# Kernel optimization log

Hardware: AMD Instinct MI355X
Metric: run time of the kernel (lower is better)

## Reference

```python
import jax, jax.numpy as jnp
import numpy as np

N_NODES = 50000
N_EDGES = 800000


def setup_inputs() -> dict:
    key = jax.random.key(0)
    ks = jax.random.split(key, 6)
    x = jax.random.normal(ks[0], (N_NODES, 22), dtype=jnp.float32)
    # small weight scale to keep tanh in its linear-ish regime
    W0 = jax.random.normal(ks[1], (22, 220), dtype=jnp.float32) * 0.1
    W1 = jax.random.normal(ks[2], (220, 220), dtype=jnp.float32) * 0.05
    W2 = jax.random.normal(ks[3], (220, 220), dtype=jnp.float32) * 0.05
    W3 = jax.random.normal(ks[4], (220, 10), dtype=jnp.float32) * 0.05
    b0 = jnp.zeros((220,), jnp.float32)
    b1 = jnp.zeros((220,), jnp.float32)
    b2 = jnp.zeros((220,), jnp.float32)
    b3 = jnp.zeros((10,), jnp.float32)
    edge_index = jax.random.randint(ks[5], (2, N_EDGES), 0, N_NODES, dtype=jnp.int64)
    return {"x": x, "W0": W0, "b0": b0, "W1": W1, "b1": b1,
            "W2": W2, "b2": b2, "W3": W3, "b3": b3, "edge_index": edge_index}


def _graph_conv(h, W, b, src, dst, inv_sqrt_out, inv_sqrt_in, activation):
    # DGL GraphConv, norm='both':
    #   h' = D_in^{-1/2} * A^T * (D_out^{-1/2} * h) @ W + b
    h = h * inv_sqrt_out[:, None]          # [N, F_in]
    m = h[src]                             # gather: [E, F_in]
    agg = jax.ops.segment_sum(m, dst, num_segments=N_NODES)  # scatter-add: [N, F_in]
    agg = agg * inv_sqrt_in[:, None]
    out = agg @ W + b
    if activation is not None:
        out = activation(out)
    return out


def reference(x, W0, b0, W1, b1, W2, b2, W3, b3, edge_index):
    src, dst = edge_index[0], edge_index[1]
    ones = jnp.ones((edge_index.shape[1],), jnp.float32)
    deg_out = jax.ops.segment_sum(ones, src, num_segments=N_NODES)
    deg_in = jax.ops.segment_sum(ones, dst, num_segments=N_NODES)
    inv_sqrt_out = jax.lax.rsqrt(jnp.maximum(deg_out, 1.0))
    inv_sqrt_in = jax.lax.rsqrt(jnp.maximum(deg_in, 1.0))

    h = _graph_conv(x, W0, b0, src, dst, inv_sqrt_out, inv_sqrt_in, jnp.tanh)
    h = _graph_conv(h, W1, b1, src, dst, inv_sqrt_out, inv_sqrt_in, jnp.tanh)
    h = _graph_conv(h, W2, b2, src, dst, inv_sqrt_out, inv_sqrt_in, jnp.tanh)
    h = _graph_conv(h, W3, b3, src, dst, inv_sqrt_out, inv_sqrt_in, None)
    return h
```

## Files before the change

kernel.cpp:

```cpp
#include <hip/hip_runtime.h>
#include <math.h>

#define N_NODES 50000
#define N_EDGES 800000
#define NPAD 50176
#define HSTR 224

typedef __attribute__((ext_vector_type(8))) short short8;
typedef __attribute__((ext_vector_type(4))) float f32x4;
typedef __attribute__((ext_vector_type(4))) _Float16 half4;


__device__ __forceinline__ float fast_tanh(float x) {
    float e = __expf(2.0f * x);
    float r = __builtin_amdgcn_rcpf(e + 1.0f);
    return 1.0f - 2.0f * r;
}

__device__ __forceinline__ unsigned short rne_bf16(float x) {
    unsigned u = __builtin_bit_cast(unsigned, x);
    return (unsigned short)((u + 0x7FFFu + ((u >> 16) & 1u)) >> 16);
}

__device__ __forceinline__ void split_bf16(float x, unsigned short& hi, unsigned short& lo) {
    hi = rne_bf16(x);
    float hf = __builtin_bit_cast(float, (unsigned)hi << 16);
    lo = rne_bf16(x - hf);
}

__device__ __forceinline__ f32x4 mfma16(short8 a, short8 b, f32x4 c) {
    return __builtin_amdgcn_mfma_f32_16x16x32_bf16(a, b, c, 0, 0, 0);
}

__device__ __forceinline__ void wsplit_one(const float* __restrict__ W, int KIN, int LDA,
                                           unsigned short* __restrict__ WT_hi,
                                           unsigned short* __restrict__ WT_lo, int idx) {
    int n = idx / LDA;
    int k = idx - n * LDA;
    float v = (n < 220 && k < KIN) ? W[k * 220 + n] : 0.f;
    unsigned short hi, lo;
    split_bf16(v, hi, lo);
    WT_hi[idx] = hi;
    WT_lo[idx] = lo;
}


__global__ void k_hist_wsplit(const int* __restrict__ ei, int* __restrict__ deg_out,
                              int* __restrict__ ecsbuf, int* __restrict__ rank,
                              const float* __restrict__ W0, const float* __restrict__ W1,
                              const float* __restrict__ W2,
                              unsigned short* __restrict__ wt0h, unsigned short* __restrict__ wt0l,
                              unsigned short* __restrict__ wt1h, unsigned short* __restrict__ wt1l,
                              unsigned short* __restrict__ wt2h, unsigned short* __restrict__ wt2l) {
    int bx = blockIdx.x;
    if (bx < 3125) {
        int e = bx * 256 + threadIdx.x;
        if (e < N_EDGES) {
            atomicAdd(&deg_out[ei[e]], 1);
            rank[e] = atomicAdd(&ecsbuf[1 + ei[N_EDGES + e]], 1);
        }
    } else if (bx < 3153) {
        int idx = (bx - 3125) * 256 + threadIdx.x;
        if (idx < 224 * 32) wsplit_one(W0, 22, 32, wt0h, wt0l, idx);
    } else if (bx < 3349) {
        int idx = (bx - 3153) * 256 + threadIdx.x;
        wsplit_one(W1, 220, 224, wt1h, wt1l, idx);
    } else {
        int idx = (bx - 3349) * 256 + threadIdx.x;
        wsplit_one(W2, 220, 224, wt2h, wt2l, idx);
    }
}

__global__ void k_scan1(const int* __restrict__ in, int* __restrict__ out,
                        int* __restrict__ bsum, int n) {
    __shared__ int s[256];
    int i = blockIdx.x * 256 + threadIdx.x;
    int v = (i < n) ? in[i] : 0;
    s[threadIdx.x] = v;
    __syncthreads();
    for (int off = 1; off < 256; off <<= 1) {
        int t = (threadIdx.x >= off) ? s[threadIdx.x - off] : 0;
        __syncthreads();
        s[threadIdx.x] += t;
        __syncthreads();
    }
    if (i < n) out[i] = s[threadIdx.x] - v;
    if (threadIdx.x == 255 && bsum) bsum[blockIdx.x] = s[255];
}

__global__ void k_scan_mid(int* __restrict__ a, int n) {
    __shared__ int s[256];
    __shared__ int carry;
    if (threadIdx.x == 0) carry = 0;
    for (int base = 0; base < n; base += 256) {
        int i = base + threadIdx.x;
        int v = (i < n) ? a[i] : 0;
        s[threadIdx.x] = v;
        __syncthreads();
        for (int off = 1; off < 256; off <<= 1) {
            int t = (threadIdx.x >= off) ? s[threadIdx.x - off] : 0;
            __syncthreads();
            s[threadIdx.x] += t;
            __syncthreads();
        }
        int c = carry;
        if (i < n) a[i] = s[threadIdx.x] - v + c;
        __syncthreads();
        if (threadIdx.x == 0) carry = c + s[255];
        __syncthreads();
    }
}

__global__ void k_scan3(int* __restrict__ out, const int* __restrict__ bscan, int n) {
    int i = blockIdx.x * 256 + threadIdx.x;
    if (i < n) out[i] += bscan[blockIdx.x];
}

__global__ void k_post_scan(const int* __restrict__ ei, const int* __restrict__ ecsbuf,
                            const int* __restrict__ rank, const int* __restrict__ deg_out,
                            const float* __restrict__ x,
                            float* __restrict__ inv_out, float* __restrict__ inv_in,
                            int* __restrict__ src_sorted, float* __restrict__ xs) {
    int bx = blockIdx.x;
    if (bx < 196) {
        int n = bx * 256 + threadIdx.x;
        if (n >= N_NODES) return;
        int di = ecsbuf[n + 2] - ecsbuf[n + 1];
        int a = deg_out[n]; if (a < 1) a = 1;
        if (di < 1) di = 1;
        inv_out[n] = 1.0f / sqrtf((float)a);
        inv_in[n]  = 1.0f / sqrtf((float)di);
    } else if (bx < 3321) {
        int e = (bx - 196) * 256 + threadIdx.x;
        if (e < N_EDGES) {
            int d = ei[N_EDGES + e];
            src_sorted[ecsbuf[1 + d] + rank[e]] = ei[e];
        }
    } else {
        int idx = (bx - 3321) * 256 + threadIdx.x;
        if (idx >= N_NODES * 11) return;
        int n = idx / 11;
        int f2 = idx - n * 11;
        int a = deg_out[n]; if (a < 1) a = 1;
        float sc = 1.0f / sqrtf((float)a);
        float2 v = *(const float2*)&x[n * 22 + f2 * 2];
        v.x *= sc; v.y *= sc;
        *(float2*)&xs[n * 22 + f2 * 2] = v;
    }
}


__global__ void k_agg22_split(const float* __restrict__ xs,
                              const int* __restrict__ ecsbuf, const int* __restrict__ srcs,
                              const float* __restrict__ inv_in,
                              unsigned short* __restrict__ A_hi, unsigned short* __restrict__ A_lo) {
    int idx = blockIdx.x * 256 + threadIdx.x;
    int n = idx >> 4, f2 = idx & 15;
    if (n >= N_NODES) return;
    float ax = 0.f, ay = 0.f;
    if (f2 <= 10) {
        const float2* xb = (const float2*)(xs) + f2;
        int e = ecsbuf[n + 1], end = ecsbuf[n + 2];
        for (; e + 3 < end; e += 4) {
            int s0 = srcs[e], s1 = srcs[e + 1], s2 = srcs[e + 2], s3 = srcs[e + 3];
            float2 v0 = xb[s0 * 11], v1 = xb[s1 * 11];
            float2 v2 = xb[s2 * 11], v3 = xb[s3 * 11];
            ax += (v0.x + v1.x) + (v2.x + v3.x);
            ay += (v0.y + v1.y) + (v2.y + v3.y);
        }
        for (; e < end; ++e) {
            float2 v0 = xb[srcs[e] * 11];
            ax += v0.x;
            ay += v0.y;
        }
        float si = inv_in[n];
        ax *= si; ay *= si;
    }
    ushort2 h2, l2;
    split_bf16(ax, h2.x, l2.x);
    split_bf16(ay, h2.y, l2.y);
    *(ushort2*)&A_hi[n * 32 + f2 * 2] = h2;
    *(ushort2*)&A_lo[n * 32 + f2 * 2] = l2;
}

__global__ __launch_bounds__(256) void k_agg220_split(const _Float16* __restrict__ h,
                                                      const int* __restrict__ ecsbuf,
                                                      const int* __restrict__ srcs,
                                                      const float* __restrict__ inv_in,
                                                      unsigned short* __restrict__ A_hi,
                                                      unsigned short* __restrict__ A_lo) {
    int lane = threadIdx.x & 63;
    int n = blockIdx.x * 4 + (threadIdx.x >> 6);
    if (n >= N_NODES || lane >= 56) return;
    size_t ob = (size_t)n * 224 + lane * 4;
    if (lane == 55) {
        ushort4 z = {0, 0, 0, 0};
        *(ushort4*)&A_hi[ob] = z;
        *(ushort4*)&A_lo[ob] = z;
        return;
    }
    int f4 = lane * 4;
    const _Float16* hb = h + f4;
    int e = ecsbuf[n + 1], end = ecsbuf[n + 2];
    float4 a0 = {0,0,0,0}, a1 = {0,0,0,0}, a2 = {0,0,0,0}, a3 = {0,0,0,0};
    for (; e + 7 < end; e += 8) {
        int s0 = srcs[e],     s1 = srcs[e + 1], s2 = srcs[e + 2], s3 = srcs[e + 3];
        int s4 = srcs[e + 4], s5 = srcs[e + 5], s6 = srcs[e + 6], s7 = srcs[e + 7];
        half4 v0 = *(const half4*)(hb + (size_t)s0 * HSTR);
        half4 v1 = *(const half4*)(hb + (size_t)s1 * HSTR);
        half4 v2 = *(const half4*)(hb + (size_t)s2 * HSTR);
        half4 v3 = *(const half4*)(hb + (size_t)s3 * HSTR);
        half4 v4 = *(const half4*)(hb + (size_t)s4 * HSTR);
        half4 v5 = *(const half4*)(hb + (size_t)s5 * HSTR);
        half4 v6 = *(const half4*)(hb + (size_t)s6 * HSTR);
        half4 v7 = *(const half4*)(hb + (size_t)s7 * HSTR);
        a0.x += (float)v0.x; a0.y += (float)v0.y; a0.z += (float)v0.z; a0.w += (float)v0.w;
        a1.x += (float)v1.x; a1.y += (float)v1.y; a1.z += (float)v1.z; a1.w += (float)v1.w;
        a2.x += (float)v2.x; a2.y += (float)v2.y; a2.z += (float)v2.z; a2.w += (float)v2.w;
        a3.x += (float)v3.x; a3.y += (float)v3.y; a3.z += (float)v3.z; a3.w += (float)v3.w;
        a0.x += (float)v4.x; a0.y += (float)v4.y; a0.z += (float)v4.z; a0.w += (float)v4.w;
        a1.x += (float)v5.x; a1.y += (float)v5.y; a1.z += (float)v5.z; a1.w += (float)v5.w;
        a2.x += (float)v6.x; a2.y += (float)v6.y; a2.z += (float)v6.z; a2.w += (float)v6.w;
        a3.x += (float)v7.x; a3.y += (float)v7.y; a3.z += (float)v7.z; a3.w += (float)v7.w;
    }
    for (; e + 3 < end; e += 4) {
        int s0 = srcs[e], s1 = srcs[e + 1], s2 = srcs[e + 2], s3 = srcs[e + 3];
        half4 v0 = *(const half4*)(hb + (size_t)s0 * HSTR);
        half4 v1 = *(const half4*)(hb + (size_t)s1 * HSTR);
        half4 v2 = *(const half4*)(hb + (size_t)s2 * HSTR);
        half4 v3 = *(const half4*)(hb + (size_t)s3 * HSTR);
        a0.x += (float)v0.x; a0.y += (float)v0.y; a0.z += (float)v0.z; a0.w += (float)v0.w;
        a1.x += (float)v1.x; a1.y += (float)v1.y; a1.z += (float)v1.z; a1.w += (float)v1.w;
        a2.x += (float)v2.x; a2.y += (float)v2.y; a2.z += (float)v2.z; a2.w += (float)v2.w;
        a3.x += (float)v3.x; a3.y += (float)v3.y; a3.z += (float)v3.z; a3.w += (float)v3.w;
    }
    for (; e < end; ++e) {
        half4 v = *(const half4*)(hb + (size_t)srcs[e] * HSTR);
        a0.x += (float)v.x; a0.y += (float)v.y; a0.z += (float)v.z; a0.w += (float)v.w;
    }
    float sc = inv_in[n];
    float4 t;
    t.x = ((a0.x + a1.x) + (a2.x + a3.x)) * sc;
    t.y = ((a0.y + a1.y) + (a2.y + a3.y)) * sc;
    t.z = ((a0.z + a1.z) + (a2.z + a3.z)) * sc;
    t.w = ((a0.w + a1.w) + (a2.w + a3.w)) * sc;
    ushort4 h4, l4;
    split_bf16(t.x, h4.x, l4.x);
    split_bf16(t.y, h4.y, l4.y);
    split_bf16(t.z, h4.z, l4.z);
    split_bf16(t.w, h4.w, l4.w);
    *(ushort4*)&A_hi[ob] = h4;
    *(ushort4*)&A_lo[ob] = l4;
}

__global__ void k_agg10_epi(const float* __restrict__ tmp, const int* __restrict__ ecsbuf,
                            const int* __restrict__ srcs, const float* __restrict__ inv_in,
                            const float* __restrict__ bias, float* __restrict__ out) {
    int idx = blockIdx.x * 256 + threadIdx.x;
    if (idx >= N_NODES * 5) return;
    int n = idx / 5;
    int f2 = idx - n * 5;
    const float2* tb = (const float2*)(tmp) + f2;
    float ax = 0.f, ay = 0.f;
    int e = ecsbuf[n + 1], end = ecsbuf[n + 2];
    for (; e + 1 < end; e += 2) {
        float2 v0 = tb[srcs[e] * 5];
        float2 v1 = tb[srcs[e + 1] * 5];
        ax += v0.x + v1.x;
        ay += v0.y + v1.y;
    }
    if (e < end) {
        float2 v0 = tb[srcs[e] * 5];
        ax += v0.x;
        ay += v0.y;
    }
    float si = inv_in[n];
    float2 o;
    o.x = ax * si + bias[f2 * 2];
    o.y = ay * si + bias[f2 * 2 + 1];
    *(float2*)&out[n * 10 + f2 * 2] = o;
}

template <int KSTEPS, int LDA, bool FUSE_W3>
__global__ __launch_bounds__(256) void k_gemm_mfma(const unsigned short* __restrict__ A_hi,
                                                   const unsigned short* __restrict__ A_lo,
                                                   const unsigned short* __restrict__ WT_hi,
                                                   const unsigned short* __restrict__ WT_lo,
                                                   const float* __restrict__ bias,
                                                   const float* __restrict__ post,
                                                   _Float16* __restrict__ out,
                                                   const float* __restrict__ W3,
                                                   float* __restrict__ tmp) {
    int tid = threadIdx.x;
    int l = tid & 63, w = tid >> 6;
    int lrow = l & 15, q = l >> 4;
    int rt = blockIdx.x * 128 + w * 32;

    const unsigned short* pa0h = A_hi + (size_t)(rt + lrow) * LDA + q * 8;
    const unsigned short* pa0l = A_lo + (size_t)(rt + lrow) * LDA + q * 8;
    const unsigned short* pa1h = pa0h + 16 * LDA;
    const unsigned short* pa1l = pa0l + 16 * LDA;

    f32x4 acc0[14], acc1[14];
#pragma unroll
    for (int ct = 0; ct < 14; ++ct) {
        acc0[ct] = (f32x4){0.f, 0.f, 0.f, 0.f};
        acc1[ct] = (f32x4){0.f, 0.f, 0.f, 0.f};
    }

#pragma unroll
    for (int ks = 0; ks < KSTEPS; ++ks) {
        int k0 = ks * 32;
        short8 ah0 = *(const short8*)(const void*)(pa0h + k0);
        short8 al0 = *(const short8*)(const void*)(pa0l + k0);
        short8 ah1 = *(const short8*)(const void*)(pa1h + k0);
        short8 al1 = *(const short8*)(const void*)(pa1l + k0);
#pragma unroll
        for (int ct = 0; ct < 14; ++ct) {
            size_t boff = (size_t)(ct * 16 + lrow) * LDA + q * 8 + k0;
            short8 bh = *(const short8*)(const void*)(WT_hi + boff);
            short8 bl = *(const short8*)(const void*)(WT_lo + boff);
            acc0[ct] = mfma16(ah0, bh, acc0[ct]);
            acc0[ct] = mfma16(ah0, bl, acc0[ct]);
            acc0[ct] = mfma16(al0, bh, acc0[ct]);
            acc1[ct] = mfma16(ah1, bh, acc1[ct]);
            acc1[ct] = mfma16(ah1, bl, acc1[ct]);
            acc1[ct] = mfma16(al1, bh, acc1[ct]);
        }
    }

    float pv0[4], pv1[4];
#pragma unroll
    for (int r = 0; r < 4; ++r) {
        int r0 = rt + q * 4 + r;
        int r1 = r0 + 16;
        pv0[r] = (r0 < N_NODES) ? post[r0] : 0.f;
        pv1[r] = (r1 < N_NODES) ? post[r1] : 0.f;
    }

    if (!FUSE_W3) {
#pragma unroll
        for (int ct = 0; ct < 14; ++ct) {
            int col = ct * 16 + lrow;
            if (col >= 220) continue;
            float bv = bias[col];
#pragma unroll
            for (int r = 0; r < 4; ++r) {
                int r0 = rt + q * 4 + r;
                int r1 = r0 + 16;
                if (r0 < N_NODES)
                    out[(size_t)r0 * HSTR + col] = (_Float16)(pv0[r] * fast_tanh(acc0[ct][r] + bv));
                if (r1 < N_NODES)
                    out[(size_t)r1 * HSTR + col] = (_Float16)(pv1[r] * fast_tanh(acc1[ct][r] + bv));
            }
        }
    } else {
#pragma unroll
        for (int half = 0; half < 2; ++half) {
            const f32x4* acc = half ? acc1 : acc0;
            const float* pv  = half ? pv1 : pv0;
            int rbase = rt + half * 16;
            float p[4][10];
#pragma unroll
            for (int r = 0; r < 4; ++r)
#pragma unroll
                for (int j = 0; j < 10; ++j) p[r][j] = 0.f;
#pragma unroll
            for (int ct = 0; ct < 14; ++ct) {
                int col = ct * 16 + lrow;
                bool cok = col < 220;
                float bv = cok ? bias[col] : 0.f;
                float w3v[10];
                if (cok) {
                    const float2* wp = (const float2*)&W3[col * 10];
#pragma unroll
                    for (int j2 = 0; j2 < 5; ++j2) {
                        float2 t = wp[j2];
                        w3v[2 * j2] = t.x;
                        w3v[2 * j2 + 1] = t.y;
                    }
                } else {
#pragma unroll
                    for (int j = 0; j < 10; ++j) w3v[j] = 0.f;
                }
#pragma unroll
                for (int r = 0; r < 4; ++r) {
                    float h2 = pv[r] * fast_tanh(acc[ct][r] + bv);
#pragma unroll
                    for (int j = 0; j < 10; ++j) p[r][j] += h2 * w3v[j];
                }
            }
#pragma unroll
            for (int r = 0; r < 4; ++r)
#pragma unroll
                for (int j = 0; j < 10; ++j) {
                    float v = p[r][j];
                    v += __shfl_xor(v, 1, 64);
                    v += __shfl_xor(v, 2, 64);
                    v += __shfl_xor(v, 4, 64);
                    v += __shfl_xor(v, 8, 64);
                    p[r][j] = v;
                }
            if (lrow == 0) {
#pragma unroll
                for (int r = 0; r < 4; ++r) {
                    int row = rbase + q * 4 + r;
                    if (row < N_NODES) {
#pragma unroll
                        for (int j2 = 0; j2 < 5; ++j2) {
                            float2 o = {p[r][2 * j2], p[r][2 * j2 + 1]};
                            *(float2*)&tmp[(size_t)row * 10 + 2 * j2] = o;
                        }
                    }
                }
            }
        }
    }
}


extern "C" void kernel_launch(void* const* d_in, const int* in_sizes, int n_in,
                              void* d_out, int out_size, void* d_ws, size_t ws_size,
                              hipStream_t stream) {
    const float* x  = (const float*)d_in[0];
    const float* W0 = (const float*)d_in[1];
    const float* b0 = (const float*)d_in[2];
    const float* W1 = (const float*)d_in[3];
    const float* b1 = (const float*)d_in[4];
    const float* W2 = (const float*)d_in[5];
    const float* b2 = (const float*)d_in[6];
    const float* W3 = (const float*)d_in[7];
    const float* b3 = (const float*)d_in[8];
    const int*   ei = (const int*)d_in[9];
    float* out = (float*)d_out;

    int* ws = (int*)d_ws;
    int* ecsbuf     = ws + 0;
    int* deg_out    = ws + 50432;
    int* bsumA      = ws + 100608;
    float* inv_out  = (float*)(ws + 100864);
    float* inv_in   = (float*)(ws + 151040);
    int* src_sorted = ws + 201216;
    unsigned short* wt0h = (unsigned short*)(ws + 1001216);
    unsigned short* wt0l = (unsigned short*)(ws + 1004800);
    unsigned short* wt1h = (unsigned short*)(ws + 1008384);
    unsigned short* wt1l = (unsigned short*)(ws + 1033472);
    unsigned short* wt2h = (unsigned short*)(ws + 1058560);
    unsigned short* wt2l = (unsigned short*)(ws + 1083648);
    unsigned short* ahi  = (unsigned short*)(ws + 1108736);
    unsigned short* alo  = (unsigned short*)(ws + 6728448);
    _Float16* hbuf = (_Float16*)(ws + 12348160);
    float* tmp10 = (float*)(ws + 23548160);
    int* rank    = (int*)ahi;
    float* xs    = (float*)(ws + 1108736 + 3000000);

    hipMemsetAsync(ws, 0, (size_t)100608 * sizeof(int), stream);

    k_hist_wsplit<<<3545, 256, 0, stream>>>(ei, deg_out, ecsbuf, rank,
                                            W0, W1, W2, wt0h, wt0l, wt1h, wt1l, wt2h, wt2l);
    k_scan1<<<196, 256, 0, stream>>>(ecsbuf + 1, ecsbuf + 1, bsumA, NPAD);
    k_scan_mid<<<1, 256, 0, stream>>>(bsumA, 196);
    k_scan3<<<196, 256, 0, stream>>>(ecsbuf + 1, bsumA, NPAD);
    k_post_scan<<<5470, 256, 0, stream>>>(ei, ecsbuf, rank, deg_out, x,
                                          inv_out, inv_in, src_sorted, xs);

    int gemm_grid = (NPAD + 127) / 128;
    int agg_grid  = (N_NODES + 3) / 4;

    k_agg22_split<<<(N_NODES * 16 + 255) / 256, 256, 0, stream>>>(
        xs, ecsbuf, src_sorted, inv_in, ahi, alo);
    k_gemm_mfma<1, 32, false><<<gemm_grid, 256, 0, stream>>>(
        ahi, alo, wt0h, wt0l, b0, inv_out, hbuf, nullptr, nullptr);

    k_agg220_split<<<agg_grid, 256, 0, stream>>>(hbuf, ecsbuf, src_sorted, inv_in, ahi, alo);
    k_gemm_mfma<7, 224, false><<<gemm_grid, 256, 0, stream>>>(
        ahi, alo, wt1h, wt1l, b1, inv_out, hbuf, nullptr, nullptr);

    k_agg220_split<<<agg_grid, 256, 0, stream>>>(hbuf, ecsbuf, src_sorted, inv_in, ahi, alo);
    k_gemm_mfma<7, 224, true><<<gemm_grid, 256, 0, stream>>>(
        ahi, alo, wt2h, wt2l, b2, inv_out, nullptr, W3, tmp10);

    k_agg10_epi<<<(N_NODES * 5 + 255) / 256, 256, 0, stream>>>(
        tmp10, ecsbuf, src_sorted, inv_in, b3, out);
}
```

Baseline: 467.9 us.

## Stage weight tiles in double-buffered LDS for MFMA GEMM

The GEMM kernel now loads the hi/lo bf16 weight slices cooperatively into a double-buffered shared-memory tile (224 rows by 72 shorts, padded) and has each wave read B fragments from LDS. Previously every wave loaded them directly from global memory. The next k-step is prefetched into registers while the current step's MFMAs run. This is meant to cut redundant global/L2 traffic for weights across the four waves. In exchange it adds about 64KB of LDS per block, which may reduce occupancy, and a barrier per k-step.

```diff
diff --git a/kernel.cpp b/kernel.cpp
--- a/kernel.cpp
+++ b/kernel.cpp
@@ -291,6 +291,8 @@
                                                    _Float16* __restrict__ out,
                                                    const float* __restrict__ W3,
                                                    float* __restrict__ tmp) {
+    __shared__ unsigned short Bs[2][224 * 72];
+
     int tid = threadIdx.x;
     int l = tid & 63, w = tid >> 6;
     int lrow = l & 15, q = l >> 4;
@@ -301,6 +303,29 @@
     const unsigned short* pa1h = pa0h + 16 * LDA;
     const unsigned short* pa1l = pa0l + 16 * LDA;
 
+    int sr[7], sjl[7], sjo[7];
+#pragma unroll
+    for (int i = 0; i < 7; ++i) {
+        int f = tid + 256 * i;
+        sr[i] = f >> 3;
+        int j = f & 7;
+        sjl[i] = (j & 3) * 8;
+        sjo[i] = (j >> 2);
+    }
+
+    {
+        short8 sreg[7];
+#pragma unroll
+        for (int i = 0; i < 7; ++i) {
+            const unsigned short* g = (sjo[i] ? WT_lo : WT_hi) + (size_t)sr[i] * LDA + sjl[i];
+            sreg[i] = *(const short8*)(const void*)g;
+        }
+#pragma unroll
+        for (int i = 0; i < 7; ++i)
+            *(short8*)(void*)&Bs[0][sr[i] * 72 + sjo[i] * 32 + sjl[i]] = sreg[i];
+    }
+    __syncthreads();
+
     f32x4 acc0[14], acc1[14];
 #pragma unroll
     for (int ct = 0; ct < 14; ++ct) {
@@ -308,24 +333,47 @@
         acc1[ct] = (f32x4){0.f, 0.f, 0.f, 0.f};
     }
 
+    int bro = lrow * 72 + q * 8;
+
 #pragma unroll
     for (int ks = 0; ks < KSTEPS; ++ks) {
+        int cur = ks & 1;
+        bool has_next = (ks + 1 < KSTEPS);
+
+        short8 sreg[7];
+        if (has_next) {
+            int k0n = (ks + 1) * 32;
+#pragma unroll
+            for (int i = 0; i < 7; ++i) {
+                const unsigned short* g = (sjo[i] ? WT_lo : WT_hi) + (size_t)sr[i] * LDA + k0n + sjl[i];
+                sreg[i] = *(const short8*)(const void*)g;
+            }
+        }
+
         int k0 = ks * 32;
         short8 ah0 = *(const short8*)(const void*)(pa0h + k0);
         short8 al0 = *(const short8*)(const void*)(pa0l + k0);
         short8 ah1 = *(const short8*)(const void*)(pa1h + k0);
         short8 al1 = *(const short8*)(const void*)(pa1l + k0);
+
 #pragma unroll
         for (int ct = 0; ct < 14; ++ct) {
-            size_t boff = (size_t)(ct * 16 + lrow) * LDA + q * 8 + k0;
-            short8 bh = *(const short8*)(const void*)(WT_hi + boff);
-            short8 bl = *(const short8*)(const void*)(WT_lo + boff);
+            const unsigned short* bp = &Bs[cur][ct * 1152 + bro];
+            short8 bh = *(const short8*)(const void*)bp;
+            short8 bl = *(const short8*)(const void*)(bp + 32);
             acc0[ct] = mfma16(ah0, bh, acc0[ct]);
             acc0[ct] = mfma16(ah0, bl, acc0[ct]);
             acc0[ct] = mfma16(al0, bh, acc0[ct]);
             acc1[ct] = mfma16(ah1, bh, acc1[ct]);
             acc1[ct] = mfma16(ah1, bl, acc1[ct]);
             acc1[ct] = mfma16(al1, bh, acc1[ct]);
+        }
+
+        if (has_next) {
+#pragma unroll
+            for (int i = 0; i < 7; ++i)
+                *(short8*)(void*)&Bs[1 - cur][sr[i] * 72 + sjo[i] * 32 + sjl[i]] = sreg[i];
+            __syncthreads();
         }
     }
 
```

New measurement: 465.8 us. No clear change (-0.5%).

## Split GEMM tiles into column halves to cut registers and raise occupancy

Applied to the files above, without the earlier changes.

The MFMA GEMM now gives each wave one 16-row tile over half of the output columns (7 column tiles) instead of two row tiles over all 14. The grid grows fourfold and launch bounds request 4 blocks per SM. The goal is fewer accumulator registers, higher occupancy and more blocks in flight. The fused W3 epilogue now writes two partial 10-wide outputs, one per column half, into separate buffers that the final aggregation kernel sums. In exchange, each A tile is loaded twice (once per column half) and the final gather does twice as many loads.

```diff
diff --git a/kernel.cpp b/kernel.cpp
--- a/kernel.cpp
+++ b/kernel.cpp
@@ -260,19 +260,20 @@
     if (idx >= N_NODES * 5) return;
     int n = idx / 5;
     int f2 = idx - n * 5;
-    const float2* tb = (const float2*)(tmp) + f2;
+    const float2* tb0 = (const float2*)(tmp) + f2;
+    const float2* tb1 = (const float2*)(tmp + (size_t)NPAD * 10) + f2;
     float ax = 0.f, ay = 0.f;
     int e = ecsbuf[n + 1], end = ecsbuf[n + 2];
     for (; e + 1 < end; e += 2) {
-        float2 v0 = tb[srcs[e] * 5];
-        float2 v1 = tb[srcs[e + 1] * 5];
-        ax += v0.x + v1.x;
-        ay += v0.y + v1.y;
+        float2 u0 = tb0[srcs[e] * 5],     w0 = tb1[srcs[e] * 5];
+        float2 u1 = tb0[srcs[e + 1] * 5], w1 = tb1[srcs[e + 1] * 5];
+        ax += (u0.x + w0.x) + (u1.x + w1.x);
+        ay += (u0.y + w0.y) + (u1.y + w1.y);
     }
     if (e < end) {
-        float2 v0 = tb[srcs[e] * 5];
-        ax += v0.x;
-        ay += v0.y;
+        float2 u0 = tb0[srcs[e] * 5], w0 = tb1[srcs[e] * 5];
+        ax += u0.x + w0.x;
+        ay += u0.y + w0.y;
     }
     float si = inv_in[n];
     float2 o;
@@ -282,135 +283,120 @@
 }
 
 template <int KSTEPS, int LDA, bool FUSE_W3>
-__global__ __launch_bounds__(256) void k_gemm_mfma(const unsigned short* __restrict__ A_hi,
-                                                   const unsigned short* __restrict__ A_lo,
-                                                   const unsigned short* __restrict__ WT_hi,
-                                                   const unsigned short* __restrict__ WT_lo,
-                                                   const float* __restrict__ bias,
-                                                   const float* __restrict__ post,
-                                                   _Float16* __restrict__ out,
-                                                   const float* __restrict__ W3,
-                                                   float* __restrict__ tmp) {
+__global__ __launch_bounds__(256, 4) void k_gemm_mfma(const unsigned short* __restrict__ A_hi,
+                                                      const unsigned short* __restrict__ A_lo,
+                                                      const unsigned short* __restrict__ WT_hi,
+                                                      const unsigned short* __restrict__ WT_lo,
+                                                      const float* __restrict__ bias,
+                                                      const float* __restrict__ post,
+                                                      _Float16* __restrict__ out,
+                                                      const float* __restrict__ W3,
+                                                      float* __restrict__ tmp) {
     int tid = threadIdx.x;
     int l = tid & 63, w = tid >> 6;
     int lrow = l & 15, q = l >> 4;
-    int rt = blockIdx.x * 128 + w * 32;
-
-    const unsigned short* pa0h = A_hi + (size_t)(rt + lrow) * LDA + q * 8;
-    const unsigned short* pa0l = A_lo + (size_t)(rt + lrow) * LDA + q * 8;
-    const unsigned short* pa1h = pa0h + 16 * LDA;
-    const unsigned short* pa1l = pa0l + 16 * LDA;
-
-    f32x4 acc0[14], acc1[14];
-#pragma unroll
-    for (int ct = 0; ct < 14; ++ct) {
-        acc0[ct] = (f32x4){0.f, 0.f, 0.f, 0.f};
-        acc1[ct] = (f32x4){0.f, 0.f, 0.f, 0.f};
-    }
+    int bid = blockIdx.x;
+    int ch = bid & 1;
+    int rt = (bid >> 1) * 64 + w * 16;
+    int cb = ch * 112;
+
+    const unsigned short* pah = A_hi + (size_t)(rt + lrow) * LDA + q * 8;
+    const unsigned short* pal = A_lo + (size_t)(rt + lrow) * LDA + q * 8;
+    const unsigned short* pbh = WT_hi + (size_t)(cb + lrow) * LDA + q * 8;
+    const unsigned short* pbl = WT_lo + (size_t)(cb + lrow) * LDA + q * 8;
+
+    f32x4 acc[7];
+#pragma unroll
+    for (int ct = 0; ct < 7; ++ct) acc[ct] = (f32x4){0.f, 0.f, 0.f, 0.f};
 
 #pragma unroll
     for (int ks = 0; ks < KSTEPS; ++ks) {
         int k0 = ks * 32;
-        short8 ah0 = *(const short8*)(const void*)(pa0h + k0);
-        short8 al0 = *(const short8*)(const void*)(pa0l + k0);
-        short8 ah1 = *(const short8*)(const void*)(pa1h + k0);
-        short8 al1 = *(const short8*)(const void*)(pa1l + k0);
-#pragma unroll
-        for (int ct = 0; ct < 14; ++ct) {
-            size_t boff = (size_t)(ct * 16 + lrow) * LDA + q * 8 + k0;
-            short8 bh = *(const short8*)(const void*)(WT_hi + boff);
-            short8 bl = *(const short8*)(const void*)(WT_lo + boff);
-            acc0[ct] = mfma16(ah0, bh, acc0[ct]);
-            acc0[ct] = mfma16(ah0, bl, acc0[ct]);
-            acc0[ct] = mfma16(al0, bh, acc0[ct]);
-            acc1[ct] = mfma16(ah1, bh, acc1[ct]);
-            acc1[ct] = mfma16(ah1, bl, acc1[ct]);
-            acc1[ct] = mfma16(al1, bh, acc1[ct]);
-        }
-    }
-
-    float pv0[4], pv1[4];
+        short8 ah = *(const short8*)(const void*)(pah + k0);
+        short8 al = *(const short8*)(const void*)(pal + k0);
+#pragma unroll
+        for (int ct = 0; ct < 7; ++ct) {
+            size_t boff = (size_t)(ct * 16) * LDA + k0;
+            short8 bh = *(const short8*)(const void*)(pbh + boff);
+            short8 bl = *(const short8*)(const void*)(pbl + boff);
+            acc[ct] = mfma16(ah, bh, acc[ct]);
+            acc[ct] = mfma16(ah, bl, acc[ct]);
+            acc[ct] = mfma16(al, bh, acc[ct]);
+        }
+    }
+
+    float pv[4];
 #pragma unroll
     for (int r = 0; r < 4; ++r) {
         int r0 = rt + q * 4 + r;
-        int r1 = r0 + 16;
-        pv0[r] = (r0 < N_NODES) ? post[r0] : 0.f;
-        pv1[r] = (r1 < N_NODES) ? post[r1] : 0.f;
+        pv[r] = (r0 < N_NODES) ? post[r0] : 0.f;
     }
 
     if (!FUSE_W3) {
 #pragma unroll
-        for (int ct = 0; ct < 14; ++ct) {
-            int col = ct * 16 + lrow;
+        for (int ct = 0; ct < 7; ++ct) {
+            int col = cb + ct * 16 + lrow;
             if (col >= 220) continue;
             float bv = bias[col];
 #pragma unroll
             for (int r = 0; r < 4; ++r) {
                 int r0 = rt + q * 4 + r;
-                int r1 = r0 + 16;
                 if (r0 < N_NODES)
-                    out[(size_t)r0 * HSTR + col] = (_Float16)(pv0[r] * fast_tanh(acc0[ct][r] + bv));
-                if (r1 < N_NODES)
-                    out[(size_t)r1 * HSTR + col] = (_Float16)(pv1[r] * fast_tanh(acc1[ct][r] + bv));
+                    out[(size_t)r0 * HSTR + col] = (_Float16)(pv[r] * fast_tanh(acc[ct][r] + bv));
             }
         }
     } else {
-#pragma unroll
-        for (int half = 0; half < 2; ++half) {
-            const f32x4* acc = half ? acc1 : acc0;
-            const float* pv  = half ? pv1 : pv0;
-            int rbase = rt + half * 16;
-            float p[4][10];
-#pragma unroll
-            for (int r = 0; r < 4; ++r)
-#pragma unroll
-                for (int j = 0; j < 10; ++j) p[r][j] = 0.f;
-#pragma unroll
-            for (int ct = 0; ct < 14; ++ct) {
-                int col = ct * 16 + lrow;
-                bool cok = col < 220;
-                float bv = cok ? bias[col] : 0.f;
-                float w3v[10];
-                if (cok) {
-                    const float2* wp = (const float2*)&W3[col * 10];
+        float p[4][10];
+#pragma unroll
+        for (int r = 0; r < 4; ++r)
+#pragma unroll
+            for (int j = 0; j < 10; ++j) p[r][j] = 0.f;
+#pragma unroll
+        for (int ct = 0; ct < 7; ++ct) {
+            int col = cb + ct * 16 + lrow;
+            bool cok = col < 220;
+            float bv = cok ? bias[col] : 0.f;
+            float w3v[10];
+            if (cok) {
+                const float2* wp = (const float2*)&W3[col * 10];
+#pragma unroll
+                for (int j2 = 0; j2 < 5; ++j2) {
+                    float2 t = wp[j2];
+                    w3v[2 * j2] = t.x;
+                    w3v[2 * j2 + 1] = t.y;
+                }
+            } else {
+#pragma unroll
+                for (int j = 0; j < 10; ++j) w3v[j] = 0.f;
+            }
+#pragma unroll
+            for (int r = 0; r < 4; ++r) {
+                float h2 = pv[r] * fast_tanh(acc[ct][r] + bv);
+#pragma unroll
+                for (int j = 0; j < 10; ++j) p[r][j] += h2 * w3v[j];
+            }
+        }
+#pragma unroll
+        for (int r = 0; r < 4; ++r)
+#pragma unroll
+            for (int j = 0; j < 10; ++j) {
+                float v = p[r][j];
+                v += __shfl_xor(v, 1, 64);
+                v += __shfl_xor(v, 2, 64);
+                v += __shfl_xor(v, 4, 64);
+                v += __shfl_xor(v, 8, 64);
+                p[r][j] = v;
+            }
+        if (lrow == 0) {
+#pragma unroll
+            for (int r = 0; r < 4; ++r) {
+                int row = rt + q * 4 + r;
+                if (row < N_NODES) {
+                    float* tp = tmp + ((size_t)ch * NPAD + row) * 10;
 #pragma unroll
                     for (int j2 = 0; j2 < 5; ++j2) {
-                        float2 t = wp[j2];
-                        w3v[2 * j2] = t.x;
-                        w3v[2 * j2 + 1] = t.y;
-                    }
-                } else {
-#pragma unroll
-                    for (int j = 0; j < 10; ++j) w3v[j] = 0.f;
-                }
-#pragma unroll
-                for (int r = 0; r < 4; ++r) {
-                    float h2 = pv[r] * fast_tanh(acc[ct][r] + bv);
-#pragma unroll
-                    for (int j = 0; j < 10; ++j) p[r][j] += h2 * w3v[j];
-                }
-            }
-#pragma unroll
-            for (int r = 0; r < 4; ++r)
-#pragma unroll
-                for (int j = 0; j < 10; ++j) {
-                    float v = p[r][j];
-                    v += __shfl_xor(v, 1, 64);
-                    v += __shfl_xor(v, 2, 64);
-                    v += __shfl_xor(v, 4, 64);
-                    v += __shfl_xor(v, 8, 64);
-                    p[r][j] = v;
-                }
-            if (lrow == 0) {
-#pragma unroll
-                for (int r = 0; r < 4; ++r) {
-                    int row = rbase + q * 4 + r;
-                    if (row < N_NODES) {
-#pragma unroll
-                        for (int j2 = 0; j2 < 5; ++j2) {
-                            float2 o = {p[r][2 * j2], p[r][2 * j2 + 1]};
-                            *(float2*)&tmp[(size_t)row * 10 + 2 * j2] = o;
-                        }
+                        float2 o = {p[r][2 * j2], p[r][2 * j2 + 1]};
+                        *(float2*)&tp[2 * j2] = o;
                     }
                 }
             }
@@ -450,7 +436,7 @@
     unsigned short* ahi  = (unsigned short*)(ws + 1108736);
     unsigned short* alo  = (unsigned short*)(ws + 6728448);
     _Float16* hbuf = (_Float16*)(ws + 12348160);
-    float* tmp10 = (float*)(ws + 23548160);
+    float* tmp10 = (float*)(ws + 17948160);
     int* rank    = (int*)ahi;
     float* xs    = (float*)(ws + 1108736 + 3000000);
 
@@ -464,7 +450,7 @@
     k_post_scan<<<5470, 256, 0, stream>>>(ei, ecsbuf, rank, deg_out, x,
                                           inv_out, inv_in, src_sorted, xs);
 
-    int gemm_grid = (NPAD + 127) / 128;
+    int gemm_grid = (NPAD / 64) * 2;
     int agg_grid  = (N_NODES + 3) / 4;
 
     k_agg22_split<<<(N_NODES * 16 + 255) / 256, 256, 0, stream>>>(
```

After: 465.8 us. About the same (-0.5%).
